# Performance work log

Measured on AMD Instinct MI355X. Metric: run time of the kernel, lower is better.

## Reference

```python
import jax, jax.numpy as jnp
import numpy as np

NODE = 100   # sensors per graph
BATCH = 64
DIM = 128    # embed dim == gnn out channels
IN_DIM = 5
TOPK = 30
INTER = 256  # out_layer hidden
EPS = 1e-5   # BatchNorm eps
SLOPE = 0.2  # leaky relu negative slope


def setup_inputs() -> dict:
    key = jax.random.key(0)
    ks = jax.random.split(key, 16)
    d = {
        "x": jax.random.normal(ks[0], (BATCH * NODE, IN_DIM), jnp.float32),
        "emb": jax.random.normal(ks[1], (NODE, DIM), jnp.float32) * 0.1,
        "w_lin": jax.random.normal(ks[2], (DIM, IN_DIM), jnp.float32) * (1.0 / np.sqrt(IN_DIM)),
        "att_i": jax.random.normal(ks[3], (DIM,), jnp.float32) * (1.0 / np.sqrt(DIM)),
        "att_j": jax.random.normal(ks[4], (DIM,), jnp.float32) * (1.0 / np.sqrt(DIM)),
        "att_em_i": jax.random.normal(ks[5], (DIM,), jnp.float32) * (1.0 / np.sqrt(DIM)),
        "att_em_j": jax.random.normal(ks[6], (DIM,), jnp.float32) * (1.0 / np.sqrt(DIM)),
        "g_bias": jax.random.normal(ks[7], (DIM,), jnp.float32) * 0.02,
        "bn1_g": jnp.ones((DIM,), jnp.float32),
        "bn1_b": jnp.zeros((DIM,), jnp.float32),
        "bn2_g": jnp.ones((DIM,), jnp.float32),
        "bn2_b": jnp.zeros((DIM,), jnp.float32),
        "bn3_g": jnp.ones((INTER,), jnp.float32),
        "bn3_b": jnp.zeros((INTER,), jnp.float32),
        "w1": jax.random.normal(ks[8], (INTER, DIM), jnp.float32) * (1.0 / np.sqrt(DIM)),
        "b1": jnp.zeros((INTER,), jnp.float32),
        "w2": jax.random.normal(ks[9], (1, INTER), jnp.float32) * (1.0 / np.sqrt(INTER)),
        "b2": jnp.zeros((1,), jnp.float32),
        "topk": TOPK,
    }
    return d


def _bn(z, g, b, axes):
    # BatchNorm1d in training mode: biased batch stats per channel (last axis)
    mu = z.mean(axes, keepdims=True)
    var = z.var(axes, keepdims=True)
    return (z - mu) / jnp.sqrt(var + EPS) * g + b


def reference(x, emb, w_lin, att_i, att_j, att_em_i, att_em_j, g_bias,
              bn1_g, bn1_b, bn2_g, bn2_b, bn3_g, bn3_b, w1, b1, w2, b2, topk):
    n, d = emb.shape
    nb = x.shape[0]            # batch*node rows
    bsz = nb // n

    # --- learned graph from cosine similarity of (detached) embeddings ---
    w = jax.lax.stop_gradient(emb)
    nrm = jnp.linalg.norm(w, axis=-1)
    cos = (w @ w.T) / (nrm[:, None] * nrm[None, :])
    _, idx = jax.lax.top_k(cos, topk)              # [n, k] neighbors j per target i
    src = idx.reshape(-1)                          # gated_j (source)
    dst = jnp.repeat(jnp.arange(n), topk)          # gated_i (target)
    off = (jnp.arange(bsz) * n)[:, None]
    src_b = (src[None, :] + off).reshape(-1)       # [bsz*n*k]
    dst_b = (dst[None, :] + off).reshape(-1)

    # --- GraphLayer: lin + gather + edge attention + segment softmax + scatter-add ---
    h = x @ w_lin.T                                # [nb, d]
    x_i = h[dst_b]
    x_j = h[src_b]
    emb_i = emb[dst_b % n]                         # all_embeddings repeated per batch
    emb_j = emb[src_b % n]
    alpha = x_i @ att_i + emb_i @ att_em_i + x_j @ att_j + emb_j @ att_em_j  # [E]
    alpha = jnp.where(alpha > 0, alpha, SLOPE * alpha)
    # segment softmax keyed by target node
    m = jax.ops.segment_max(alpha, dst_b, num_segments=nb)
    a = jnp.exp(alpha - m[dst_b])
    s = jax.ops.segment_sum(a, dst_b, num_segments=nb)
    attw = a / (s[dst_b] + 1e-16)
    agg = jax.ops.segment_sum(x_j * attw[:, None], dst_b, num_segments=nb) + g_bias

    # GNNLayer: BN + ReLU
    y = jax.nn.relu(_bn(agg, bn1_g, bn1_b, 0))     # [nb, d]

    # --- GDN head ---
    x3 = y.reshape(bsz, n, d) * emb[None]          # mul with node embeddings
    x3 = jax.nn.relu(_bn(x3, bn2_g, bn2_b, (0, 1)))
    # OutLayer: Linear -> BN -> ReLU -> Linear
    o = x3 @ w1.T + b1                             # [bsz, n, INTER]
    o = jax.nn.relu(_bn(o, bn3_g, bn3_b, (0, 1)))
    o = o @ w2.T + b2                              # [bsz, n, 1]
    return o.reshape(-1, 1)
```

## Files before the change

### kernel.cpp

```cpp
#include <hip/hip_runtime.h>

#define NODE 100
#define BATCH 64
#define DIM 128
#define IN_DIM 5
#define TOPK 30
#define INTER 256
#define NB (BATCH*NODE)
#define EPS 1e-5f
#define SLOPE 0.2f
#define REP 16
#define NBLK 400
#define ROWS 16
#define NTHR 512
#define GRPS 16
#define GRPSZ (NBLK/GRPS)

#define OFF_AGG    0
#define OFF_X3     819200
#define OFF_O1     1638400
#define OFF_U      3276800
#define OFF_EI     3276816
#define OFF_EJ     3276928
#define OFF_STATA  3277056
#define OFF_STAT2  3277568
#define OFF_STAT3  3281664
#define OFF_BAR    3289856
#define OFF_IDX    3294208
#define ZERO_BYTES ((OFF_IDX - OFF_STATA) * 4)

__device__ __forceinline__ float aload(const float* p) {
    return __hip_atomic_load(p, __ATOMIC_RELAXED, __HIP_MEMORY_SCOPE_AGENT);
}
__device__ __forceinline__ void astore(float* p, float v) {
    __hip_atomic_store(p, v, __ATOMIC_RELAXED, __HIP_MEMORY_SCOPE_AGENT);
}
__device__ __forceinline__ int aloadi(const int* p) {
    return __hip_atomic_load(p, __ATOMIC_RELAXED, __HIP_MEMORY_SCOPE_AGENT);
}
__device__ __forceinline__ void astorei(int* p, int v) {
    __hip_atomic_store(p, v, __ATOMIC_RELAXED, __HIP_MEMORY_SCOPE_AGENT);
}

__device__ __forceinline__ void gbar(int* base) {
    __syncthreads();
    if (threadIdx.x == 0) {
        int g = blockIdx.x & (GRPS-1);
        int* sub  = base + g*64;
        int* root = base + 1024;
        int* flag = base + 1025;
        int v = __hip_atomic_fetch_add(sub, 1, __ATOMIC_RELAXED, __HIP_MEMORY_SCOPE_AGENT);
        if (v == GRPSZ-1) {
            int r = __hip_atomic_fetch_add(root, 1, __ATOMIC_RELAXED, __HIP_MEMORY_SCOPE_AGENT);
            if (r == GRPS-1)
                __hip_atomic_store(flag, 1, __ATOMIC_RELAXED, __HIP_MEMORY_SCOPE_AGENT);
        }
        while (!__hip_atomic_load(flag, __ATOMIC_RELAXED, __HIP_MEMORY_SCOPE_AGENT))
            __builtin_amdgcn_s_sleep(1);
    }
    __syncthreads();
}

__global__ __launch_bounds__(NTHR, 4) void k_fused(
        const float* __restrict__ x, const float* __restrict__ emb,
        const float* __restrict__ w_lin,
        const float* __restrict__ att_i, const float* __restrict__ att_j,
        const float* __restrict__ att_em_i, const float* __restrict__ att_em_j,
        const float* __restrict__ g_bias,
        const float* __restrict__ g1, const float* __restrict__ b1,
        const float* __restrict__ g2, const float* __restrict__ b2v,
        const float* __restrict__ g3, const float* __restrict__ b3,
        const float* __restrict__ w1, const float* __restrict__ b1v,
        const float* __restrict__ w2, const float* __restrict__ b2s,
        float* __restrict__ ws, int* __restrict__ idx, float* __restrict__ out) {
    __shared__ __align__(16) float smem[13504];
    int* bar = (int*)(ws + OFF_BAR);
    const int b = blockIdx.x, t = threadIdx.x, w = t >> 6, l = t & 63;
    const float invn = 1.f/(float)NB;
    const int r0 = b * ROWS;
    const int fb = r0 / NODE, lb = (r0 + ROWS - 1) / NODE;

    if (b < 13) {
        float* eT = smem;
        int i = b*8 + w;
        bool act = (i < NODE);
        int j0 = l, j1 = l + 64;
        bool ok1 = (j1 < NODE);
        float d0 = 0.f, d1 = 0.f, ni = 0.f, n0 = 0.f, n1 = 0.f;
        for (int kc = 0; kc < 4; ++kc) {
            __syncthreads();
            for (int ii = t; ii < 3200; ii += NTHR) {
                int n = ii >> 5, d = ii & 31;
                eT[d*101 + n] = emb[n*DIM + kc*32 + d];
            }
            __syncthreads();
            if (act) {
#pragma unroll
                for (int dd = 0; dd < 32; ++dd) {
                    float ei = eT[dd*101 + i];
                    float a0 = eT[dd*101 + j0];
                    ni += ei*ei; d0 += ei*a0; n0 += a0*a0;
                    if (ok1) { float a1v = eT[dd*101 + j1]; d1 += ei*a1v; n1 += a1v*a1v; }
                }
            }
        }
        if (act) {
            float sni = sqrtf(ni);
            float c0 = d0 / (sni * sqrtf(n0));
            float c1 = ok1 ? d1 / (sni * sqrtf(n1)) : -INFINITY;
            for (int r = 0; r < TOPK; ++r) {
                float bv; int bi;
                if (c1 > c0) { bv = c1; bi = j1; } else { bv = c0; bi = j0; }
#pragma unroll
                for (int m = 32; m >= 1; m >>= 1) {
                    float ov = __shfl_xor(bv, m, 64);
                    int   oi = __shfl_xor(bi, m, 64);
                    if (ov > bv || (ov == bv && oi < bi)) { bv = ov; bi = oi; }
                }
                if (l == 0) astorei(idx + i*TOPK + r, bi);
                if (bi == j0) c0 = -INFINITY;
                if (bi == j1) c1 = -INFINITY;
            }
        }
    } else if (b == 13) {
        float* Pi = smem;
        float* Pj = smem + 640;
        if (t < DIM) {
            float wi = att_i[t], wj = att_j[t];
#pragma unroll
            for (int c = 0; c < IN_DIM; ++c) {
                float wl = w_lin[t*IN_DIM + c];
                Pi[c*128 + t] = wl*wi;
                Pj[c*128 + t] = wl*wj;
            }
        }
        __syncthreads();
        if (t < 10) {
            int c = (t < 5) ? t : t - 5;
            const float* P = (t < 5) ? Pi : Pj;
            float s = 0.f;
            for (int k = 0; k < DIM; ++k) s += P[c*128 + k];
            astore(ws + OFF_U + t, s);
        }
        float a0 = att_em_i[l], a1 = att_em_i[l+64];
        float b0 = att_em_j[l], b1v_ = att_em_j[l+64];
        int nend = w*13 + 13; if (nend > NODE) nend = NODE;
        for (int n = w*13; n < nend; ++n) {
            float v0 = emb[n*DIM + l], v1 = emb[n*DIM + l + 64];
            float pi = v0*a0 + v1*a1;
            float pj = v0*b0 + v1*b1v_;
#pragma unroll
            for (int m = 32; m >= 1; m >>= 1) {
                pi += __shfl_xor(pi, m, 64);
                pj += __shfl_xor(pj, m, 64);
            }
            if (l == 0) { astore(ws + OFF_EI + n, pi); astore(ws + OFF_EJ + n, pj); }
        }
    } else {
        float* xl = smem + 16;
        for (int i = t; i < 500; i += NTHR) {
            xl[i]       = x[fb*500 + i];
            xl[500 + i] = x[lb*500 + i];
        }
    }
    gbar(bar);

    {
        float* ul   = smem;
        float* xl   = smem + 16;
        float* sjl  = smem + 1016;
        float* eil  = smem + 1216;
        int*   idl  = (int*)(smem + 1232);
        float* psum = smem + 1712;
        float* agg  = ws + OFF_AGG;
        if (b < 14) {
            for (int i = t; i < 500; i += NTHR) {
                xl[i]       = x[fb*500 + i];
                xl[500 + i] = x[lb*500 + i];
            }
        }
        if (t < 10) ul[t] = aload(ws + OFF_U + t);
        if (t < ROWS) eil[t] = aload(ws + OFF_EI + (r0 + t) % NODE);
        if (t < ROWS*TOPK)
            idl[t] = aloadi(idx + ((r0 + t/TOPK) % NODE)*TOPK + t % TOPK);
        __syncthreads();
        if (t < 200) {
            int bb = t / 100, n = t % 100;
            float s = aload(ws + OFF_EJ + n);
#pragma unroll
            for (int c = 0; c < IN_DIM; ++c) s += xl[bb*500 + n*IN_DIM + c] * ul[5 + c];
            sjl[t] = s;
        }
        __syncthreads();
        float wl0[IN_DIM], wl1[IN_DIM];
#pragma unroll
        for (int c = 0; c < IN_DIM; ++c) {
            wl0[c] = w_lin[l*IN_DIM + c];
            wl1[c] = w_lin[(l+64)*IN_DIM + c];
        }
        float gb0 = g_bias[l], gb1 = g_bias[l+64];
        float S0=0,S1=0,S2=0,S3=0,S4=0;
        float M[15];
#pragma unroll
        for (int m = 0; m < 15; ++m) M[m] = 0.f;
        for (int rr = w; rr < ROWS; rr += 8) {
            int row = r0 + rr;
            int bb = (row / NODE == fb) ? 0 : 1;
            int node = row % NODE;
            float si = eil[rr];
#pragma unroll
            for (int c = 0; c < IN_DIM; ++c) si += xl[bb*500 + node*IN_DIM + c] * ul[c];
            float mx = -INFINITY;
#pragma unroll
            for (int r = 0; r < TOPK; ++r) {
                int s = idl[rr*TOPK + r];
                float a = si + sjl[bb*100 + s];
                a = (a > 0.f) ? a : SLOPE*a;
                mx = fmaxf(mx, a);
            }
            float ssum = 0.f, x0=0,x1=0,x2=0,x3v=0,x4=0;
#pragma unroll
            for (int r = 0; r < TOPK; ++r) {
                int s = idl[rr*TOPK + r];
                float a = si + sjl[bb*100 + s];
                a = (a > 0.f) ? a : SLOPE*a;
                float e = expf(a - mx);
                ssum += e;
                const float* xr = &xl[bb*500 + s*IN_DIM];
                x0 += e*xr[0]; x1 += e*xr[1]; x2 += e*xr[2]; x3v += e*xr[3]; x4 += e*xr[4];
            }
            float inv = 1.f/(ssum + 1e-16f);
            float y0=x0*inv, y1=x1*inv, y2=x2*inv, y3=x3v*inv, y4=x4*inv;
            float o0 = y0*wl0[0]+y1*wl0[1]+y2*wl0[2]+y3*wl0[3]+y4*wl0[4] + gb0;
            float o1 = y0*wl1[0]+y1*wl1[1]+y2*wl1[2]+y3*wl1[3]+y4*wl1[4] + gb1;
            agg[row*DIM + l]      = o0;
            agg[row*DIM + l + 64] = o1;
            S0+=y0; S1+=y1; S2+=y2; S3+=y3; S4+=y4;
            M[0]+=y0*y0; M[1]+=y0*y1; M[2]+=y0*y2; M[3]+=y0*y3; M[4]+=y0*y4;
            M[5]+=y1*y1; M[6]+=y1*y2; M[7]+=y1*y3; M[8]+=y1*y4;
            M[9]+=y2*y2; M[10]+=y2*y3; M[11]+=y2*y4;
            M[12]+=y3*y3; M[13]+=y3*y4; M[14]+=y4*y4;
        }
        __syncthreads();
        if (l == 0) {
            psum[w*20+0]=S0; psum[w*20+1]=S1; psum[w*20+2]=S2; psum[w*20+3]=S3; psum[w*20+4]=S4;
#pragma unroll
            for (int m = 0; m < 15; ++m) psum[w*20+5+m] = M[m];
        }
        __syncthreads();
        if (t < 20) {
            float p = 0.f;
#pragma unroll
            for (int q = 0; q < 8; ++q) p += psum[q*20 + t];
            atomicAdd(&ws[OFF_STATA + (b & (REP-1))*32 + t], p);
        }
    }
    gbar(bar + 1088);

    {
        float* A  = smem;
        float* pv = smem + 32;
        float* pq = smem + 2080;
        if (t < 20) {
            float s = 0.f;
#pragma unroll
            for (int r = 0; r < REP; ++r) s += aload(ws + OFF_STATA + r*32 + t);
            A[t] = s;
        }
        __syncthreads();
        int cq = (t & 31) * 4;
        float muq[4], rsg[4], bq[4];
#pragma unroll
        for (int q = 0; q < 4; ++q) {
            int c = cq + q;
            float w0 = w_lin[c*IN_DIM+0], w1v = w_lin[c*IN_DIM+1], w2v = w_lin[c*IN_DIM+2],
                  w3 = w_lin[c*IN_DIM+3], w4 = w_lin[c*IN_DIM+4];
            float Sv = A[0]*w0 + A[1]*w1v + A[2]*w2v + A[3]*w3 + A[4]*w4;
            float Q  = w0*w0*A[5] + w1v*w1v*A[10] + w2v*w2v*A[14] + w3*w3*A[17] + w4*w4*A[19]
                     + 2.f*(w0*w1v*A[6] + w0*w2v*A[7] + w0*w3*A[8] + w0*w4*A[9]
                          + w1v*w2v*A[11] + w1v*w3*A[12] + w1v*w4*A[13]
                          + w2v*w3*A[15] + w2v*w4*A[16] + w3*w4*A[18]);
            float mv = Sv*invn;
            float mu = mv + g_bias[c];
            float var = fmaxf(Q*invn - mv*mv, 0.f);
            float rs = rsqrtf(var + EPS);
            muq[q] = mu; rsg[q] = rs*g1[c]; bq[q] = b1[c];
        }
        const float4* agg4 = (const float4*)(ws + OFF_AGG);
        const float4* emb4 = (const float4*)emb;
        float4* x34 = (float4*)(ws + OFF_X3);
        int i4 = b*512 + t;
        int row = i4 >> 5;
        int node = row % NODE;
        float4 av = agg4[i4];
        float4 ev = emb4[node*32 + (t & 31)];
        float o[4];
#pragma unroll
        for (int q = 0; q < 4; ++q) {
            float val = (((const float*)&av)[q] - muq[q])*rsg[q] + bq[q];
            val = fmaxf(val, 0.f);
            o[q] = val * ((const float*)&ev)[q];
        }
        x34[i4] = make_float4(o[0], o[1], o[2], o[3]);
        int g = t >> 5;
        *(float4*)&pv[g*128 + cq] = make_float4(o[0], o[1], o[2], o[3]);
        *(float4*)&pq[g*128 + cq] = make_float4(o[0]*o[0], o[1]*o[1], o[2]*o[2], o[3]*o[3]);
        __syncthreads();
        if (t < DIM) {
            float s1 = 0.f, s2 = 0.f;
#pragma unroll
            for (int r = 0; r < 16; ++r) { s1 += pv[r*128 + t]; s2 += pq[r*128 + t]; }
            atomicAdd(&ws[OFF_STAT2 + (b & (REP-1))*256 + t], s1);
            atomicAdd(&ws[OFF_STAT2 + (b & (REP-1))*256 + DIM + t], s2);
        }
    }
    gbar(bar + 2*1088);

    {
        float* aT     = smem;
        float* wT     = smem + 576;
        float* ps     = smem + 8896;
        float* ps2    = smem + 10944;
        float* bn2raw = smem + 12992;
        float* mu2l   = smem + 13248;
        float* rs2l   = smem + 13376;
        if (t < 256) {
            float s = 0.f;
#pragma unroll
            for (int r = 0; r < REP; ++r) s += aload(ws + OFF_STAT2 + r*256 + t);
            bn2raw[t] = s;
        }
        __syncthreads();
        if (t < DIM) {
            float mu = bn2raw[t]*invn;
            float var = fmaxf(bn2raw[DIM + t]*invn - mu*mu, 0.f);
            mu2l[t] = mu;
            rs2l[t] = rsqrtf(var + EPS);
        }
        __syncthreads();
        const float* x3 = ws + OFF_X3;
        float* o1 = ws + OFF_O1;
        int cg = t & 63;
        int rg = t >> 6;
        float acc[2][4];
#pragma unroll
        for (int a = 0; a < 2; ++a)
#pragma unroll
            for (int q = 0; q < 4; ++q) acc[a][q] = 0.f;
        int kk = t & 31;
        for (int k0 = 0; k0 < DIM; k0 += 32) {
            {
                int row = t >> 5;
                int k = k0 + kk;
                float v = (x3[(r0+row)*DIM + k] - mu2l[k])*rs2l[k]*g2[k] + b2v[k];
                aT[row*36 + kk] = fmaxf(v, 0.f);
            }
            for (int i = t; i < 8192; i += NTHR) {
                int kk2 = i & 31, c = i >> 5;
                wT[kk2*260 + c] = w1[c*DIM + k0 + kk2];
            }
            __syncthreads();
#pragma unroll
            for (int q4 = 0; q4 < 8; ++q4) {
                float4 av[2], wv[4];
#pragma unroll
                for (int rr = 0; rr < 2; ++rr)
                    av[rr] = *(const float4*)&aT[(rg*2+rr)*36 + q4*4];
#pragma unroll
                for (int q = 0; q < 4; ++q)
                    wv[q] = *(const float4*)&wT[(q4*4+q)*260 + cg*4];
#pragma unroll
                for (int rr = 0; rr < 2; ++rr) {
                    acc[rr][0] += av[rr].x*wv[0].x + av[rr].y*wv[1].x + av[rr].z*wv[2].x + av[rr].w*wv[3].x;
                    acc[rr][1] += av[rr].x*wv[0].y + av[rr].y*wv[1].y + av[rr].z*wv[2].y + av[rr].w*wv[3].y;
                    acc[rr][2] += av[rr].x*wv[0].z + av[rr].y*wv[1].z + av[rr].z*wv[2].z + av[rr].w*wv[3].z;
                    acc[rr][3] += av[rr].x*wv[0].w + av[rr].y*wv[1].w + av[rr].z*wv[2].w + av[rr].w*wv[3].w;
                }
            }
            __syncthreads();
        }
        int cbase = cg*4;
        float4 bv = *(const float4*)&b1v[cbase];
        float lv[4]  = {0,0,0,0};
        float lv2[4] = {0,0,0,0};
#pragma unroll
        for (int rr = 0; rr < 2; ++rr) {
            int row = r0 + rg*2 + rr;
            float o0 = acc[rr][0] + bv.x;
            float o1v = acc[rr][1] + bv.y;
            float o2 = acc[rr][2] + bv.z;
            float o3 = acc[rr][3] + bv.w;
            *(float4*)&o1[row*INTER + cbase] = make_float4(o0, o1v, o2, o3);
            lv[0]+=o0;  lv2[0]+=o0*o0;
            lv[1]+=o1v; lv2[1]+=o1v*o1v;
            lv[2]+=o2;  lv2[2]+=o2*o2;
            lv[3]+=o3;  lv2[3]+=o3*o3;
        }
        *(float4*)&ps[rg*256 + cbase]  = make_float4(lv[0], lv[1], lv[2], lv[3]);
        *(float4*)&ps2[rg*256 + cbase] = make_float4(lv2[0], lv2[1], lv2[2], lv2[3]);
        __syncthreads();
        if (t < INTER) {
            float s1 = 0.f, s2 = 0.f;
#pragma unroll
            for (int q = 0; q < 8; ++q) { s1 += ps[q*256 + t]; s2 += ps2[q*256 + t]; }
            atomicAdd(&ws[OFF_STAT3 + (b & (REP-1))*512 + t], s1);
            atomicAdd(&ws[OFF_STAT3 + (b & (REP-1))*512 + INTER + t], s2);
        }
    }
    gbar(bar + 3*1088);

    {
        float* raw  = smem;
        float* mu3l = smem + 512;
        float* rs3l = smem + 768;
        {
            float s = 0.f;
#pragma unroll
            for (int r = 0; r < REP; ++r) s += aload(ws + OFF_STAT3 + r*512 + t);
            raw[t] = s;
        }
        __syncthreads();
        if (t < INTER) {
            float mu = raw[t]*invn;
            float var = fmaxf(raw[256 + t]*invn - mu*mu, 0.f);
            mu3l[t] = mu;
            rs3l[t] = rsqrtf(var + EPS);
        }
        __syncthreads();
        float m3[4], rg3[4], b3q[4], w2q[4];
#pragma unroll
        for (int q = 0; q < 4; ++q) {
            int c = l*4 + q;
            m3[q] = mu3l[c];
            rg3[q] = rs3l[c]*g3[c];
            b3q[q] = b3[c];
            w2q[q] = w2[c];
        }
        float bias2 = b2s[0];
        const float4* o14 = (const float4*)(ws + OFF_O1);
#pragma unroll
        for (int j = 0; j < 2; ++j) {
            int row = r0 + w*2 + j;
            float4 vv = o14[row*64 + l];
            float s = 0.f;
#pragma unroll
            for (int q = 0; q < 4; ++q) {
                float val = (((const float*)&vv)[q] - m3[q])*rg3[q] + b3q[q];
                val = fmaxf(val, 0.f);
                s += val * w2q[q];
            }
#pragma unroll
            for (int m = 32; m >= 1; m >>= 1) s += __shfl_xor(s, m, 64);
            if (l == 0) out[row] = s + bias2;
        }
    }
}

extern "C" void kernel_launch(void* const* d_in, const int* in_sizes, int n_in,
                              void* d_out, int out_size, void* d_ws, size_t ws_size,
                              hipStream_t stream) {
    const float* x        = (const float*)d_in[0];
    const float* emb      = (const float*)d_in[1];
    const float* w_lin    = (const float*)d_in[2];
    const float* att_i    = (const float*)d_in[3];
    const float* att_j    = (const float*)d_in[4];
    const float* att_em_i = (const float*)d_in[5];
    const float* att_em_j = (const float*)d_in[6];
    const float* g_bias   = (const float*)d_in[7];
    const float* bn1_g    = (const float*)d_in[8];
    const float* bn1_b    = (const float*)d_in[9];
    const float* bn2_g    = (const float*)d_in[10];
    const float* bn2_b    = (const float*)d_in[11];
    const float* bn3_g    = (const float*)d_in[12];
    const float* bn3_b    = (const float*)d_in[13];
    const float* w1       = (const float*)d_in[14];
    const float* b1       = (const float*)d_in[15];
    const float* w2       = (const float*)d_in[16];
    const float* b2       = (const float*)d_in[17];
    float* out = (float*)d_out;
    float* ws  = (float*)d_ws;
    int*   idx = (int*)(ws + OFF_IDX);

    hipMemsetAsync((void*)(ws + OFF_STATA), 0, ZERO_BYTES, stream);

    k_fused<<<NBLK, NTHR, 0, stream>>>(x, emb, w_lin, att_i, att_j, att_em_i,
                                       att_em_j, g_bias, bn1_g, bn1_b, bn2_g, bn2_b,
                                       bn3_g, bn3_b, w1, b1, w2, b2, ws, idx, out);
}
```

Measured before the change: 182.2 us.

## Recompute graph per block and keep intermediates in shared memory, dropping one grid barrier

Each block now recomputes the top-k cosine graph rows it needs, along with the embedding projections, from a transposed shared copy of emb. This removes the first grid-wide barrier and the global idx/U/EI/EJ exchange. The agg, x3 and o1 intermediates now stay in LDS across phases instead of round-tripping through global workspace. The grid barrier also moves to per-group release flags with acquire/release ordering. The trade-offs are redundant cosine work in every block, larger shared memory use (~76KB) that may lower occupancy, and the risk of co-residency issues for the spin barrier.

```diff
diff --git a/kernel.cpp b/kernel.cpp
--- a/kernel.cpp
+++ b/kernel.cpp
@@ -16,47 +16,43 @@
 #define GRPS 16
 #define GRPSZ (NBLK/GRPS)
 
-#define OFF_AGG    0
-#define OFF_X3     819200
-#define OFF_O1     1638400
-#define OFF_U      3276800
-#define OFF_EI     3276816
-#define OFF_EJ     3276928
-#define OFF_STATA  3277056
-#define OFF_STAT2  3277568
-#define OFF_STAT3  3281664
-#define OFF_BAR    3289856
-#define OFF_IDX    3294208
-#define ZERO_BYTES ((OFF_IDX - OFF_STATA) * 4)
+#define OFF_STATA 0
+#define OFF_STAT2 512
+#define OFF_STAT3 4608
+#define OFF_BARF  12800
+#define BAR_STRIDE 4096
+#define ZERO_BYTES ((OFF_BARF + 3*BAR_STRIDE) * 4)
+
+#define R1_OFF 12800
+#define R2_OFF 14848
+#define SMEM_FL 18944
 
 __device__ __forceinline__ float aload(const float* p) {
     return __hip_atomic_load(p, __ATOMIC_RELAXED, __HIP_MEMORY_SCOPE_AGENT);
 }
-__device__ __forceinline__ void astore(float* p, float v) {
-    __hip_atomic_store(p, v, __ATOMIC_RELAXED, __HIP_MEMORY_SCOPE_AGENT);
-}
-__device__ __forceinline__ int aloadi(const int* p) {
-    return __hip_atomic_load(p, __ATOMIC_RELAXED, __HIP_MEMORY_SCOPE_AGENT);
-}
-__device__ __forceinline__ void astorei(int* p, int v) {
-    __hip_atomic_store(p, v, __ATOMIC_RELAXED, __HIP_MEMORY_SCOPE_AGENT);
-}
 
 __device__ __forceinline__ void gbar(int* base) {
     __syncthreads();
     if (threadIdx.x == 0) {
         int g = blockIdx.x & (GRPS-1);
-        int* sub  = base + g*64;
-        int* root = base + 1024;
-        int* flag = base + 1025;
-        int v = __hip_atomic_fetch_add(sub, 1, __ATOMIC_RELAXED, __HIP_MEMORY_SCOPE_AGENT);
+        int* sub   = base + g*64;
+        int* root  = base + 1024;
+        int* rflag = base + 1088;
+        int* gflag = base + 2048 + g*64;
+        int v = __hip_atomic_fetch_add(sub, 1, __ATOMIC_RELEASE, __HIP_MEMORY_SCOPE_AGENT);
         if (v == GRPSZ-1) {
-            int r = __hip_atomic_fetch_add(root, 1, __ATOMIC_RELAXED, __HIP_MEMORY_SCOPE_AGENT);
-            if (r == GRPS-1)
-                __hip_atomic_store(flag, 1, __ATOMIC_RELAXED, __HIP_MEMORY_SCOPE_AGENT);
-        }
-        while (!__hip_atomic_load(flag, __ATOMIC_RELAXED, __HIP_MEMORY_SCOPE_AGENT))
-            __builtin_amdgcn_s_sleep(1);
+            int r = __hip_atomic_fetch_add(root, 1, __ATOMIC_ACQ_REL, __HIP_MEMORY_SCOPE_AGENT);
+            if (r == GRPS-1) {
+                __hip_atomic_store(rflag, 1, __ATOMIC_RELEASE, __HIP_MEMORY_SCOPE_AGENT);
+            } else {
+                while (!__hip_atomic_load(rflag, __ATOMIC_ACQUIRE, __HIP_MEMORY_SCOPE_AGENT))
+                    __builtin_amdgcn_s_sleep(4);
+            }
+            __hip_atomic_store(gflag, 1, __ATOMIC_RELEASE, __HIP_MEMORY_SCOPE_AGENT);
+        } else {
+            while (!__hip_atomic_load(gflag, __ATOMIC_ACQUIRE, __HIP_MEMORY_SCOPE_AGENT))
+                __builtin_amdgcn_s_sleep(4);
+        }
     }
     __syncthreads();
 }
@@ -72,126 +68,92 @@
         const float* __restrict__ g3, const float* __restrict__ b3,
         const float* __restrict__ w1, const float* __restrict__ b1v,
         const float* __restrict__ w2, const float* __restrict__ b2s,
-        float* __restrict__ ws, int* __restrict__ idx, float* __restrict__ out) {
-    __shared__ __align__(16) float smem[13504];
-    int* bar = (int*)(ws + OFF_BAR);
+        float* __restrict__ ws, float* __restrict__ out) {
+    __shared__ __align__(16) float smem[SMEM_FL];
+    int* bar = (int*)(ws + OFF_BARF);
     const int b = blockIdx.x, t = threadIdx.x, w = t >> 6, l = t & 63;
     const float invn = 1.f/(float)NB;
     const int r0 = b * ROWS;
     const int fb = r0 / NODE, lb = (r0 + ROWS - 1) / NODE;
-
-    if (b < 13) {
-        float* eT = smem;
-        int i = b*8 + w;
-        bool act = (i < NODE);
-        int j0 = l, j1 = l + 64;
-        bool ok1 = (j1 < NODE);
-        float d0 = 0.f, d1 = 0.f, ni = 0.f, n0 = 0.f, n1 = 0.f;
-        for (int kc = 0; kc < 4; ++kc) {
-            __syncthreads();
-            for (int ii = t; ii < 3200; ii += NTHR) {
-                int n = ii >> 5, d = ii & 31;
-                eT[d*101 + n] = emb[n*DIM + kc*32 + d];
-            }
-            __syncthreads();
-            if (act) {
-#pragma unroll
-                for (int dd = 0; dd < 32; ++dd) {
-                    float ei = eT[dd*101 + i];
-                    float a0 = eT[dd*101 + j0];
-                    ni += ei*ei; d0 += ei*a0; n0 += a0*a0;
-                    if (ok1) { float a1v = eT[dd*101 + j1]; d1 += ei*a1v; n1 += a1v*a1v; }
-                }
-            }
-        }
-        if (act) {
-            float sni = sqrtf(ni);
-            float c0 = d0 / (sni * sqrtf(n0));
-            float c1 = ok1 ? d1 / (sni * sqrtf(n1)) : -INFINITY;
-            for (int r = 0; r < TOPK; ++r) {
-                float bv; int bi;
-                if (c1 > c0) { bv = c1; bi = j1; } else { bv = c0; bi = j0; }
-#pragma unroll
-                for (int m = 32; m >= 1; m >>= 1) {
-                    float ov = __shfl_xor(bv, m, 64);
-                    int   oi = __shfl_xor(bi, m, 64);
-                    if (ov > bv || (ov == bv && oi < bi)) { bv = ov; bi = oi; }
-                }
-                if (l == 0) astorei(idx + i*TOPK + r, bi);
-                if (bi == j0) c0 = -INFINITY;
-                if (bi == j1) c1 = -INFINITY;
-            }
-        }
-    } else if (b == 13) {
-        float* Pi = smem;
-        float* Pj = smem + 640;
-        if (t < DIM) {
-            float wi = att_i[t], wj = att_j[t];
-#pragma unroll
-            for (int c = 0; c < IN_DIM; ++c) {
-                float wl = w_lin[t*IN_DIM + c];
-                Pi[c*128 + t] = wl*wi;
-                Pj[c*128 + t] = wl*wj;
-            }
-        }
-        __syncthreads();
-        if (t < 10) {
-            int c = (t < 5) ? t : t - 5;
-            const float* P = (t < 5) ? Pi : Pj;
-            float s = 0.f;
-            for (int k = 0; k < DIM; ++k) s += P[c*128 + k];
-            astore(ws + OFF_U + t, s);
-        }
-        float a0 = att_em_i[l], a1 = att_em_i[l+64];
-        float b0 = att_em_j[l], b1v_ = att_em_j[l+64];
-        int nend = w*13 + 13; if (nend > NODE) nend = NODE;
-        for (int n = w*13; n < nend; ++n) {
-            float v0 = emb[n*DIM + l], v1 = emb[n*DIM + l + 64];
-            float pi = v0*a0 + v1*a1;
-            float pj = v0*b0 + v1*b1v_;
+    float* eT   = smem;
+    float* aggL = smem + R1_OFF;
+    float* xl   = smem + R2_OFF;
+    float* ej   = smem + R2_OFF + 1008;
+    float* nrm  = smem + R2_OFF + 1112;
+    float* sjl  = smem + R2_OFF + 1216;
+    float* eiL  = smem + R2_OFF + 1424;
+    float* uL   = smem + R2_OFF + 1440;
+    float* psum = smem + R2_OFF + 1456;
+    int*   idl  = (int*)(smem + R2_OFF + 1616);
+    float* cosL = smem + R2_OFF + 2112;
+
+    for (int i = t; i < NODE*DIM; i += NTHR) {
+        int node = i >> 7, d = i & 127;
+        eT[d*NODE + node] = emb[i];
+    }
+    for (int i = t; i < 500; i += NTHR) {
+        xl[i]       = x[fb*500 + i];
+        xl[500 + i] = x[lb*500 + i];
+    }
+    if (t < 10) {
+        int c = (t < 5) ? t : t - 5;
+        const float* P = (t < 5) ? att_i : att_j;
+        float s = 0.f;
+        for (int k = 0; k < DIM; ++k) s += w_lin[k*IN_DIM + c] * P[k];
+        uL[t] = s;
+    }
+    __syncthreads();
+    if (t < NODE) {
+        float sn = 0.f, se = 0.f;
+        for (int d = 0; d < DIM; ++d) {
+            float v = eT[d*NODE + t];
+            sn += v*v;
+            se += v * att_em_j[d];
+        }
+        nrm[t] = sn;
+        ej[t] = se;
+    } else if (t >= 128 && t < 128 + ROWS) {
+        int node = (r0 + t - 128) % NODE;
+        float s = 0.f;
+        for (int d = 0; d < DIM; ++d) s += eT[d*NODE + node] * att_em_i[d];
+        eiL[t - 128] = s;
+    }
+    __syncthreads();
+    if (t < 200) {
+        int bb = t / 100, n = t % 100;
+        float s = ej[n];
+#pragma unroll
+        for (int c = 0; c < IN_DIM; ++c) s += xl[bb*500 + n*IN_DIM + c] * uL[5 + c];
+        sjl[t] = s;
+    }
+    for (int p = t; p < ROWS*NODE; p += NTHR) {
+        int ri = p / NODE, j = p % NODE;
+        int ni = (r0 + ri) % NODE;
+        float dot = 0.f;
+        for (int d = 0; d < DIM; ++d) dot += eT[d*NODE + ni] * eT[d*NODE + j];
+        cosL[ri*101 + j] = dot / (sqrtf(nrm[ni]) * sqrtf(nrm[j]));
+    }
+    __syncthreads();
+    for (int rr = w*2; rr < w*2 + 2; ++rr) {
+        float c0 = cosL[rr*101 + l];
+        float c1 = (l < NODE - 64) ? cosL[rr*101 + 64 + l] : -INFINITY;
+        int j0 = l, j1 = 64 + l;
+        for (int r = 0; r < TOPK; ++r) {
+            float bv; int bi;
+            if (c1 > c0) { bv = c1; bi = j1; } else { bv = c0; bi = j0; }
 #pragma unroll
             for (int m = 32; m >= 1; m >>= 1) {
-                pi += __shfl_xor(pi, m, 64);
-                pj += __shfl_xor(pj, m, 64);
-            }
-            if (l == 0) { astore(ws + OFF_EI + n, pi); astore(ws + OFF_EJ + n, pj); }
-        }
-    } else {
-        float* xl = smem + 16;
-        for (int i = t; i < 500; i += NTHR) {
-            xl[i]       = x[fb*500 + i];
-            xl[500 + i] = x[lb*500 + i];
-        }
-    }
-    gbar(bar);
-
+                float ov = __shfl_xor(bv, m, 64);
+                int   oi = __shfl_xor(bi, m, 64);
+                if (ov > bv || (ov == bv && oi < bi)) { bv = ov; bi = oi; }
+            }
+            if (l == 0) idl[rr*TOPK + r] = bi;
+            if (bi == j0) c0 = -INFINITY;
+            if (bi == j1) c1 = -INFINITY;
+        }
+    }
+    __syncthreads();
     {
-        float* ul   = smem;
-        float* xl   = smem + 16;
-        float* sjl  = smem + 1016;
-        float* eil  = smem + 1216;
-        int*   idl  = (int*)(smem + 1232);
-        float* psum = smem + 1712;
-        float* agg  = ws + OFF_AGG;
-        if (b < 14) {
-            for (int i = t; i < 500; i += NTHR) {
-                xl[i]       = x[fb*500 + i];
-                xl[500 + i] = x[lb*500 + i];
-            }
-        }
-        if (t < 10) ul[t] = aload(ws + OFF_U + t);
-        if (t < ROWS) eil[t] = aload(ws + OFF_EI + (r0 + t) % NODE);
-        if (t < ROWS*TOPK)
-            idl[t] = aloadi(idx + ((r0 + t/TOPK) % NODE)*TOPK + t % TOPK);
-        __syncthreads();
-        if (t < 200) {
-            int bb = t / 100, n = t % 100;
-            float s = aload(ws + OFF_EJ + n);
-#pragma unroll
-            for (int c = 0; c < IN_DIM; ++c) s += xl[bb*500 + n*IN_DIM + c] * ul[5 + c];
-            sjl[t] = s;
-        }
-        __syncthreads();
         float wl0[IN_DIM], wl1[IN_DIM];
 #pragma unroll
         for (int c = 0; c < IN_DIM; ++c) {
@@ -207,9 +169,9 @@
             int row = r0 + rr;
             int bb = (row / NODE == fb) ? 0 : 1;
             int node = row % NODE;
-            float si = eil[rr];
-#pragma unroll
-            for (int c = 0; c < IN_DIM; ++c) si += xl[bb*500 + node*IN_DIM + c] * ul[c];
+            float si = eiL[rr];
+#pragma unroll
+            for (int c = 0; c < IN_DIM; ++c) si += xl[bb*500 + node*IN_DIM + c] * uL[c];
             float mx = -INFINITY;
 #pragma unroll
             for (int r = 0; r < TOPK; ++r) {
@@ -231,10 +193,8 @@
             }
             float inv = 1.f/(ssum + 1e-16f);
             float y0=x0*inv, y1=x1*inv, y2=x2*inv, y3=x3v*inv, y4=x4*inv;
-            float o0 = y0*wl0[0]+y1*wl0[1]+y2*wl0[2]+y3*wl0[3]+y4*wl0[4] + gb0;
-            float o1 = y0*wl1[0]+y1*wl1[1]+y2*wl1[2]+y3*wl1[3]+y4*wl1[4] + gb1;
-            agg[row*DIM + l]      = o0;
-            agg[row*DIM + l + 64] = o1;
+            aggL[rr*DIM + l]      = y0*wl0[0]+y1*wl0[1]+y2*wl0[2]+y3*wl0[3]+y4*wl0[4] + gb0;
+            aggL[rr*DIM + l + 64] = y0*wl1[0]+y1*wl1[1]+y2*wl1[2]+y3*wl1[3]+y4*wl1[4] + gb1;
             S0+=y0; S1+=y1; S2+=y2; S3+=y3; S4+=y4;
             M[0]+=y0*y0; M[1]+=y0*y1; M[2]+=y0*y2; M[3]+=y0*y3; M[4]+=y0*y4;
             M[5]+=y1*y1; M[6]+=y1*y2; M[7]+=y1*y3; M[8]+=y1*y4;
@@ -255,75 +215,64 @@
             atomicAdd(&ws[OFF_STATA + (b & (REP-1))*32 + t], p);
         }
     }
-    gbar(bar + 1088);
+    gbar(bar);
 
     {
-        float* A  = smem;
-        float* pv = smem + 32;
-        float* pq = smem + 2080;
+        float* pv  = smem + R2_OFF;
+        float* pq  = smem + R2_OFF + 512;
+        float* A20 = smem + R2_OFF + 1024;
         if (t < 20) {
             float s = 0.f;
 #pragma unroll
             for (int r = 0; r < REP; ++r) s += aload(ws + OFF_STATA + r*32 + t);
-            A[t] = s;
-        }
-        __syncthreads();
-        int cq = (t & 31) * 4;
-        float muq[4], rsg[4], bq[4];
-#pragma unroll
-        for (int q = 0; q < 4; ++q) {
-            int c = cq + q;
-            float w0 = w_lin[c*IN_DIM+0], w1v = w_lin[c*IN_DIM+1], w2v = w_lin[c*IN_DIM+2],
-                  w3 = w_lin[c*IN_DIM+3], w4 = w_lin[c*IN_DIM+4];
-            float Sv = A[0]*w0 + A[1]*w1v + A[2]*w2v + A[3]*w3 + A[4]*w4;
-            float Q  = w0*w0*A[5] + w1v*w1v*A[10] + w2v*w2v*A[14] + w3*w3*A[17] + w4*w4*A[19]
-                     + 2.f*(w0*w1v*A[6] + w0*w2v*A[7] + w0*w3*A[8] + w0*w4*A[9]
-                          + w1v*w2v*A[11] + w1v*w3*A[12] + w1v*w4*A[13]
-                          + w2v*w3*A[15] + w2v*w4*A[16] + w3*w4*A[18]);
-            float mv = Sv*invn;
-            float mu = mv + g_bias[c];
-            float var = fmaxf(Q*invn - mv*mv, 0.f);
-            float rs = rsqrtf(var + EPS);
-            muq[q] = mu; rsg[q] = rs*g1[c]; bq[q] = b1[c];
-        }
-        const float4* agg4 = (const float4*)(ws + OFF_AGG);
-        const float4* emb4 = (const float4*)emb;
-        float4* x34 = (float4*)(ws + OFF_X3);
-        int i4 = b*512 + t;
-        int row = i4 >> 5;
-        int node = row % NODE;
-        float4 av = agg4[i4];
-        float4 ev = emb4[node*32 + (t & 31)];
-        float o[4];
-#pragma unroll
-        for (int q = 0; q < 4; ++q) {
-            float val = (((const float*)&av)[q] - muq[q])*rsg[q] + bq[q];
+            A20[t] = s;
+        }
+        __syncthreads();
+        int c = t & 127;
+        float w0 = w_lin[c*IN_DIM+0], w1v = w_lin[c*IN_DIM+1], w2v = w_lin[c*IN_DIM+2],
+              w3 = w_lin[c*IN_DIM+3], w4 = w_lin[c*IN_DIM+4];
+        float Sv = A20[0]*w0 + A20[1]*w1v + A20[2]*w2v + A20[3]*w3 + A20[4]*w4;
+        float Q  = w0*w0*A20[5] + w1v*w1v*A20[10] + w2v*w2v*A20[14] + w3*w3*A20[17] + w4*w4*A20[19]
+                 + 2.f*(w0*w1v*A20[6] + w0*w2v*A20[7] + w0*w3*A20[8] + w0*w4*A20[9]
+                      + w1v*w2v*A20[11] + w1v*w3*A20[12] + w1v*w4*A20[13]
+                      + w2v*w3*A20[15] + w2v*w4*A20[16] + w3*w4*A20[18]);
+        float mv = Sv*invn;
+        float mu = mv + g_bias[c];
+        float var = fmaxf(Q*invn - mv*mv, 0.f);
+        float rsg = rsqrtf(var + EPS) * g1[c];
+        float bq = b1[c];
+        float s1 = 0.f, s2 = 0.f;
+#pragma unroll
+        for (int k = 0; k < 4; ++k) {
+            int e = t + k*NTHR;
+            int row = e >> 7;
+            int node = (r0 + row) % NODE;
+            float val = (aggL[e] - mu)*rsg + bq;
             val = fmaxf(val, 0.f);
-            o[q] = val * ((const float*)&ev)[q];
-        }
-        x34[i4] = make_float4(o[0], o[1], o[2], o[3]);
-        int g = t >> 5;
-        *(float4*)&pv[g*128 + cq] = make_float4(o[0], o[1], o[2], o[3]);
-        *(float4*)&pq[g*128 + cq] = make_float4(o[0]*o[0], o[1]*o[1], o[2]*o[2], o[3]*o[3]);
+            float x3v = val * eT[c*NODE + node];
+            aggL[e] = x3v;
+            s1 += x3v; s2 += x3v*x3v;
+        }
+        pv[(t>>7)*128 + c] = s1;
+        pq[(t>>7)*128 + c] = s2;
         __syncthreads();
         if (t < DIM) {
-            float s1 = 0.f, s2 = 0.f;
-#pragma unroll
-            for (int r = 0; r < 16; ++r) { s1 += pv[r*128 + t]; s2 += pq[r*128 + t]; }
-            atomicAdd(&ws[OFF_STAT2 + (b & (REP-1))*256 + t], s1);
-            atomicAdd(&ws[OFF_STAT2 + (b & (REP-1))*256 + DIM + t], s2);
-        }
-    }
-    gbar(bar + 2*1088);
+            float a1 = pv[t] + pv[128+t] + pv[256+t] + pv[384+t];
+            float a2 = pq[t] + pq[128+t] + pq[256+t] + pq[384+t];
+            atomicAdd(&ws[OFF_STAT2 + (b & (REP-1))*256 + t], a1);
+            atomicAdd(&ws[OFF_STAT2 + (b & (REP-1))*256 + DIM + t], a2);
+        }
+    }
+    gbar(bar + BAR_STRIDE);
 
     {
-        float* aT     = smem;
-        float* wT     = smem + 576;
-        float* ps     = smem + 8896;
-        float* ps2    = smem + 10944;
-        float* bn2raw = smem + 12992;
-        float* mu2l   = smem + 13248;
-        float* rs2l   = smem + 13376;
+        float* bn2raw = smem + R2_OFF;
+        float* mu2l   = smem + R2_OFF + 256;
+        float* rs2l   = smem + R2_OFF + 384;
+        float* wT     = smem;
+        float* ps     = smem + 8320;
+        float* ps2    = smem + 10368;
+        float* o1L    = smem + R2_OFF;
         if (t < 256) {
             float s = 0.f;
 #pragma unroll
@@ -338,26 +287,27 @@
             rs2l[t] = rsqrtf(var + EPS);
         }
         __syncthreads();
-        const float* x3 = ws + OFF_X3;
-        float* o1 = ws + OFF_O1;
-        int cg = t & 63;
-        int rg = t >> 6;
+        {
+            int c = t & 127;
+            float mu = mu2l[c], rs = rs2l[c], gg = g2[c], bb = b2v[c];
+#pragma unroll
+            for (int k = 0; k < 4; ++k) {
+                int e = t + k*NTHR;
+                float v = (aggL[e] - mu)*rs*gg + bb;
+                aggL[e] = fmaxf(v, 0.f);
+            }
+        }
+        __syncthreads();
+        int cg = t & 63, rg = t >> 6;
         float acc[2][4];
 #pragma unroll
         for (int a = 0; a < 2; ++a)
 #pragma unroll
             for (int q = 0; q < 4; ++q) acc[a][q] = 0.f;
-        int kk = t & 31;
         for (int k0 = 0; k0 < DIM; k0 += 32) {
-            {
-                int row = t >> 5;
-                int k = k0 + kk;
-                float v = (x3[(r0+row)*DIM + k] - mu2l[k])*rs2l[k]*g2[k] + b2v[k];
-                aT[row*36 + kk] = fmaxf(v, 0.f);
-            }
             for (int i = t; i < 8192; i += NTHR) {
-                int kk2 = i & 31, c = i >> 5;
-                wT[kk2*260 + c] = w1[c*DIM + k0 + kk2];
+                int kk2 = i & 31, col = i >> 5;
+                wT[kk2*260 + col] = w1[col*DIM + k0 + kk2];
             }
             __syncthreads();
 #pragma unroll
@@ -365,7 +315,7 @@
                 float4 av[2], wv[4];
 #pragma unroll
                 for (int rr = 0; rr < 2; ++rr)
-                    av[rr] = *(const float4*)&aT[(rg*2+rr)*36 + q4*4];
+                    av[rr] = *(const float4*)&aggL[(rg*2+rr)*DIM + k0 + q4*4];
 #pragma unroll
                 for (int q = 0; q < 4; ++q)
                     wv[q] = *(const float4*)&wT[(q4*4+q)*260 + cg*4];
@@ -385,12 +335,12 @@
         float lv2[4] = {0,0,0,0};
 #pragma unroll
         for (int rr = 0; rr < 2; ++rr) {
-            int row = r0 + rg*2 + rr;
+            int row = rg*2 + rr;
             float o0 = acc[rr][0] + bv.x;
             float o1v = acc[rr][1] + bv.y;
             float o2 = acc[rr][2] + bv.z;
             float o3 = acc[rr][3] + bv.w;
-            *(float4*)&o1[row*INTER + cbase] = make_float4(o0, o1v, o2, o3);
+            *(float4*)&o1L[row*INTER + cbase] = make_float4(o0, o1v, o2, o3);
             lv[0]+=o0;  lv2[0]+=o0*o0;
             lv[1]+=o1v; lv2[1]+=o1v*o1v;
             lv[2]+=o2;  lv2[2]+=o2*o2;
@@ -407,12 +357,13 @@
             atomicAdd(&ws[OFF_STAT3 + (b & (REP-1))*512 + INTER + t], s2);
         }
     }
-    gbar(bar + 3*1088);
+    gbar(bar + 2*BAR_STRIDE);
 
     {
         float* raw  = smem;
         float* mu3l = smem + 512;
         float* rs3l = smem + 768;
+        float* o1L  = smem + R2_OFF;
         {
             float s = 0.f;
 #pragma unroll
@@ -437,11 +388,10 @@
             w2q[q] = w2[c];
         }
         float bias2 = b2s[0];
-        const float4* o14 = (const float4*)(ws + OFF_O1);
 #pragma unroll
         for (int j = 0; j < 2; ++j) {
-            int row = r0 + w*2 + j;
-            float4 vv = o14[row*64 + l];
+            int row = w*2 + j;
+            float4 vv = *(const float4*)&o1L[row*INTER + l*4];
             float s = 0.f;
 #pragma unroll
             for (int q = 0; q < 4; ++q) {
@@ -451,7 +401,7 @@
             }
 #pragma unroll
             for (int m = 32; m >= 1; m >>= 1) s += __shfl_xor(s, m, 64);
-            if (l == 0) out[row] = s + bias2;
+            if (l == 0) out[r0 + row] = s + bias2;
         }
     }
 }
@@ -479,11 +429,10 @@
     const float* b2       = (const float*)d_in[17];
     float* out = (float*)d_out;
     float* ws  = (float*)d_ws;
-    int*   idx = (int*)(ws + OFF_IDX);
-
-    hipMemsetAsync((void*)(ws + OFF_STATA), 0, ZERO_BYTES, stream);
+
+    hipMemsetAsync(d_ws, 0, ZERO_BYTES, stream);
 
     k_fused<<<NBLK, NTHR, 0, stream>>>(x, emb, w_lin, att_i, att_j, att_em_i,
                                        att_em_j, g_bias, bn1_g, bn1_b, bn2_g, bn2_b,
-                                       bn3_g, bn3_b, w1, b1, w2, b2, ws, idx, out);
+                                       bn3_g, bn3_b, w1, b1, w2, b2, ws, out);
 }
```

Measured after the change: 296.8 us. +62.9%, slower.
